# Kernel optimization log

Measured on AMD Instinct MI355X. Metric: run time of the kernel, lower is better.

Reference implementation:

```python
import jax, jax.numpy as jnp
import numpy as np

D_MODEL = 1024
N_HEADS = 16
D_K = D_MODEL // N_HEADS  # 64, also d_v
B, S = 8, 1024


def setup_inputs() -> dict:
    key = jax.random.key(0)
    ks = jax.random.split(key, 12)
    sc = 1.0 / np.sqrt(D_MODEL)
    inp = {
        "q": jax.random.normal(ks[0], (B, S, D_MODEL), jnp.float32),
        "k": jax.random.normal(ks[1], (B, S, D_MODEL), jnp.float32),
        "v": jax.random.normal(ks[2], (B, S, D_MODEL), jnp.float32),
        # per-head projection weights stacked over heads; torch Linear stores [out,in]
        "Wq": jax.random.normal(ks[3], (N_HEADS, D_K, D_MODEL), jnp.float32) * sc,
        "bq": jax.random.normal(ks[4], (N_HEADS, D_K), jnp.float32) * sc,
        "Wk": jax.random.normal(ks[5], (N_HEADS, D_K, D_MODEL), jnp.float32) * sc,
        "bk": jax.random.normal(ks[6], (N_HEADS, D_K), jnp.float32) * sc,
        "Wv": jax.random.normal(ks[7], (N_HEADS, D_K, D_MODEL), jnp.float32) * sc,
        "bv": jax.random.normal(ks[8], (N_HEADS, D_K), jnp.float32) * sc,
        "Wf": jax.random.normal(ks[9], (D_MODEL, D_MODEL), jnp.float32) * sc,
        "bf": jax.random.normal(ks[10], (D_MODEL,), jnp.float32) * sc,
    }
    return inp


def reference(q, k, v, Wq, bq, Wk, bk, Wv, bv, Wf, bf):
    temper = jnp.asarray(D_K ** 0.5, q.dtype)
    # per-head linear projections, all heads at once: [b,s,h,dk]
    qh = jnp.einsum('bsd,hkd->bhsk', q, Wq) + bq[None, :, None, :]
    kh = jnp.einsum('bsd,hkd->bhsk', k, Wk) + bk[None, :, None, :]
    vh = jnp.einsum('bsd,hkd->bhsk', v, Wv) + bv[None, :, None, :]
    # scaled dot-product scores [b,h,s,s]
    scores = jnp.einsum('bhik,bhjk->bhij', qh, kh) / temper
    # faithful scalar-equality mask: positions exactly equal to mask (=0) -> -inf
    scores = jnp.where(scores == 0.0, -jnp.inf, scores)
    attn = jax.nn.softmax(scores, axis=-1)
    out = jnp.einsum('bhij,bhjv->bhiv', attn, vh)  # [b,h,s,dv]
    # concat heads (head order matches torch.cat over ModuleList)
    out = out.transpose(0, 2, 1, 3).reshape(out.shape[0], out.shape[2], -1)  # [b,s,d_model]
    return out @ Wf.T + bf
```

## Files before the change

kernel.cpp:

```cpp
#include <hip/hip_runtime.h>
#include <hip/hip_bf16.h>


#define D_MODEL_ 1024
#define NH_ 16
#define DK_ 64
#define B_ 8
#define S_ 1024
#define M_ (B_ * S_)

typedef __hip_bfloat16 bf16;
typedef __attribute__((ext_vector_type(8))) short short8;
typedef __attribute__((ext_vector_type(4))) short short4_t;
typedef __attribute__((ext_vector_type(4))) float f32x4;

typedef const __attribute__((address_space(1))) unsigned int* gas_u32p;
typedef __attribute__((address_space(3))) unsigned int* las_u32p;

__device__ __forceinline__ short f2bs(float x) {
  bf16 h = __float2bfloat16(x);
  return *reinterpret_cast<short*>(&h);
}

__global__ __launch_bounds__(256)
void conv_f32_bf16(const float* __restrict__ in, bf16* __restrict__ out) {
  size_t i = ((size_t)blockIdx.x * 256 + threadIdx.x) * 8;
  f32x4 a = *(const f32x4*)(in + i);
  f32x4 b = *(const f32x4*)(in + i + 4);
  short8 s;
  s[0] = f2bs(a[0]); s[1] = f2bs(a[1]); s[2] = f2bs(a[2]); s[3] = f2bs(a[3]);
  s[4] = f2bs(b[0]); s[5] = f2bs(b[1]); s[6] = f2bs(b[2]); s[7] = f2bs(b[3]);
  *(short8*)((short*)out + i) = s;
}

__global__ __launch_bounds__(256)
void conv_w4(const float* __restrict__ w0, const float* __restrict__ w1,
             const float* __restrict__ w2, const float* __restrict__ w3,
             bf16* __restrict__ out) {
  const float* src = (blockIdx.z == 0) ? w0 : (blockIdx.z == 1) ? w1
                   : (blockIdx.z == 2) ? w2 : w3;
  size_t i = ((size_t)blockIdx.x * 256 + threadIdx.x) * 8;
  f32x4 a = *(const f32x4*)(src + i);
  f32x4 b = *(const f32x4*)(src + i + 4);
  short8 s;
  s[0] = f2bs(a[0]); s[1] = f2bs(a[1]); s[2] = f2bs(a[2]); s[3] = f2bs(a[3]);
  s[4] = f2bs(b[0]); s[5] = f2bs(b[1]); s[6] = f2bs(b[2]); s[7] = f2bs(b[3]);
  *(short8*)((short*)out + (size_t)blockIdx.z * 1024 * 1024 + i) = s;
}

__global__ __launch_bounds__(256)
void gemm_mfma(const void* __restrict__ A, const bf16* __restrict__ Wb,
               const float* __restrict__ bias, void* __restrict__ C,
               int aF32, int cMode)
{
  __shared__ short As[2][128 * 32];
  __shared__ short Bs[2][128 * 32];
  const int tid = threadIdx.x;
  const int lane = tid & 63;
  const int w = tid >> 6;
  const int l15 = lane & 15, quad = lane >> 4;
  const int wm = (w >> 1) * 64, wn = (w & 1) * 64;
  const int m0 = blockIdx.x * 128, n0 = blockIdx.y * 128;

  const int srow = (lane >> 2);
  const int skc  = (lane & 3) * 8;

  f32x4 acc[4][4];
#pragma unroll
  for (int i = 0; i < 4; ++i)
#pragma unroll
    for (int j = 0; j < 4; ++j)
      acc[i][j] = (f32x4){0.f, 0.f, 0.f, 0.f};

  for (int k0 = 0; k0 < 1024; k0 += 64) {
    __syncthreads();
    if (aF32) {
      const float* Af = (const float*)A;
#pragma unroll
      for (int p = 0; p < 4; ++p) {
        int c = p * 256 + tid;
        int r = c >> 3, kc = (c & 7) * 8;
        const float* g = Af + (size_t)(m0 + r) * 1024 + k0 + kc;
        f32x4 u = *(const f32x4*)g;
        f32x4 v = *(const f32x4*)(g + 4);
        short8 s;
        s[0] = f2bs(u[0]); s[1] = f2bs(u[1]); s[2] = f2bs(u[2]); s[3] = f2bs(u[3]);
        s[4] = f2bs(v[0]); s[5] = f2bs(v[1]); s[6] = f2bs(v[2]); s[7] = f2bs(v[3]);
        *(short8*)&As[kc >> 5][r * 32 + (kc & 31)] = s;
      }
    } else {
      const bf16* Ab = (const bf16*)A;
#pragma unroll
      for (int sub = 0; sub < 2; ++sub)
#pragma unroll
        for (int p = 0; p < 2; ++p) {
          int r = 32 * w + 16 * p + srow;
          __builtin_amdgcn_global_load_lds(
              (gas_u32p)(const void*)(Ab + (size_t)(m0 + r) * 1024 + k0 + sub * 32 + skc),
              (las_u32p)(void*)((char*)&As[sub][0] + w * 2048 + p * 1024), 16, 0, 0);
        }
    }
#pragma unroll
    for (int sub = 0; sub < 2; ++sub)
#pragma unroll
      for (int p = 0; p < 2; ++p) {
        int r = 32 * w + 16 * p + srow;
        __builtin_amdgcn_global_load_lds(
            (gas_u32p)(const void*)(Wb + (size_t)(n0 + r) * 1024 + k0 + sub * 32 + skc),
            (las_u32p)(void*)((char*)&Bs[sub][0] + w * 2048 + p * 1024), 16, 0, 0);
      }
    __syncthreads();

#pragma unroll
    for (int kk = 0; kk < 2; ++kk) {
      short8 af[4], bfv[4];
#pragma unroll
      for (int t = 0; t < 4; ++t) {
        af[t]  = *(short8*)&As[kk][(wm + t * 16 + l15) * 32 + quad * 8];
        bfv[t] = *(short8*)&Bs[kk][(wn + t * 16 + l15) * 32 + quad * 8];
      }
#pragma unroll
      for (int mt = 0; mt < 4; ++mt)
#pragma unroll
        for (int nt = 0; nt < 4; ++nt)
          acc[mt][nt] = __builtin_amdgcn_mfma_f32_16x16x32_bf16(af[mt], bfv[nt], acc[mt][nt], 0, 0, 0);
    }
  }

  if (cMode == 2) {
    bf16* vt = (bf16*)C;
    const int bidx = m0 >> 10;
    const int sbase = (m0 & 1023) + wm;
#pragma unroll
    for (int nt = 0; nt < 4; ++nt) {
      int n = n0 + wn + nt * 16 + l15;
      float bv = bias[n];
#pragma unroll
      for (int mt = 0; mt < 4; ++mt) {
        int s = sbase + mt * 16 + quad * 4;
        short4_t pk;
#pragma unroll
        for (int r = 0; r < 4; ++r) pk[r] = f2bs(acc[mt][nt][r] + bv);
        *(short4_t*)((short*)vt + ((size_t)bidx * 1024 + n) * 1024 + s) = pk;
      }
    }
  } else {
#pragma unroll
    for (int nt = 0; nt < 4; ++nt) {
      int col = n0 + wn + nt * 16 + l15;
      float bv = bias[col];
#pragma unroll
      for (int mt = 0; mt < 4; ++mt)
#pragma unroll
        for (int r = 0; r < 4; ++r) {
          int row = m0 + wm + mt * 16 + quad * 4 + r;
          float val = acc[mt][nt][r] + bv;
          if (cMode == 1) ((float*)C)[(size_t)row * 1024 + col] = val;
          else ((bf16*)C)[(size_t)row * 1024 + col] = __float2bfloat16(val);
        }
    }
  }
}

__global__ __launch_bounds__(256)
void attn_mfma(const bf16* __restrict__ QH, const bf16* __restrict__ KH,
               const bf16* __restrict__ VT, bf16* __restrict__ AO)
{
  __shared__ short Ks[2][64 * 32];
  __shared__ short Vs[2][64 * 32];
  __shared__ short Ps[4][16 * 72];
  const int tid = threadIdx.x;
  const int lane = tid & 63;
  const int w = tid >> 6;
  const int l15 = lane & 15, quad = lane >> 4;
  const int q0 = blockIdx.x * 64;
  const int h = blockIdx.y, b = blockIdx.z;
  const size_t base = ((size_t)b * S_) * D_MODEL_ + (size_t)h * DK_;
  const size_t vtb  = (((size_t)b * NH_ + h) * DK_) * (size_t)S_;
  const float NEG = -1e30f;
  short* myPs = Ps[w];

  const int srow = 16 * w + (lane >> 2);
  const int skc  = (lane & 3) * 8;

  short8 qa[2];
#pragma unroll
  for (int ks = 0; ks < 2; ++ks)
    qa[ks] = *(const short8*)((const short*)QH + base + (size_t)(q0 + w * 16 + l15) * D_MODEL_ + ks * 32 + quad * 8);

  float mi = NEG, li = 0.f;
  f32x4 oacc[4];
#pragma unroll
  for (int nt = 0; nt < 4; ++nt) oacc[nt] = (f32x4){0.f, 0.f, 0.f, 0.f};

  for (int j0 = 0; j0 < S_; j0 += 64) {
    __syncthreads();
#pragma unroll
    for (int sub = 0; sub < 2; ++sub) {
      __builtin_amdgcn_global_load_lds(
          (gas_u32p)(const void*)((const short*)KH + base + (size_t)(j0 + srow) * D_MODEL_ + sub * 32 + skc),
          (las_u32p)(void*)((char*)&Ks[sub][0] + w * 1024), 16, 0, 0);
      __builtin_amdgcn_global_load_lds(
          (gas_u32p)(const void*)((const short*)VT + vtb + (size_t)srow * S_ + j0 + sub * 32 + skc),
          (las_u32p)(void*)((char*)&Vs[sub][0] + w * 1024), 16, 0, 0);
    }
    __syncthreads();

    short8 kb[4][2], vb[4][2];
#pragma unroll
    for (int nt = 0; nt < 4; ++nt)
#pragma unroll
      for (int ks = 0; ks < 2; ++ks) {
        kb[nt][ks] = *(short8*)&Ks[ks][(nt * 16 + l15) * 32 + quad * 8];
        vb[nt][ks] = *(short8*)&Vs[ks][(nt * 16 + l15) * 32 + quad * 8];
      }

    f32x4 sacc[4];
#pragma unroll
    for (int nt = 0; nt < 4; ++nt) sacc[nt] = (f32x4){0.f, 0.f, 0.f, 0.f};
#pragma unroll
    for (int nt = 0; nt < 4; ++nt)
#pragma unroll
      for (int ks = 0; ks < 2; ++ks)
        sacc[nt] = __builtin_amdgcn_mfma_f32_16x16x32_bf16(kb[nt][ks], qa[ks], sacc[nt], 0, 0, 0);

    float p[4][4], rm = NEG;
#pragma unroll
    for (int nt = 0; nt < 4; ++nt)
#pragma unroll
      for (int r = 0; r < 4; ++r) {
        float x = sacc[nt][r] * 0.125f;
        if (x == 0.0f) x = NEG;
        p[nt][r] = x;
        rm = fmaxf(rm, x);
      }
    rm = fmaxf(rm, __shfl_xor(rm, 16, 64));
    rm = fmaxf(rm, __shfl_xor(rm, 32, 64));
    float nm = fmaxf(mi, rm);
    float alpha = __expf(mi - nm);
    float ps = 0.f;
#pragma unroll
    for (int nt = 0; nt < 4; ++nt)
#pragma unroll
      for (int r = 0; r < 4; ++r) {
        float e = __expf(p[nt][r] - nm);
        p[nt][r] = e;
        ps += e;
      }
    ps += __shfl_xor(ps, 16, 64);
    ps += __shfl_xor(ps, 32, 64);
    li = li * alpha + ps;
    mi = nm;

#pragma unroll
    for (int nt = 0; nt < 4; ++nt) {
      short4_t pk;
#pragma unroll
      for (int r = 0; r < 4; ++r) pk[r] = f2bs(p[nt][r]);
      *(short4_t*)&myPs[l15 * 72 + nt * 16 + quad * 4] = pk;
    }

    float ar[4];
#pragma unroll
    for (int r = 0; r < 4; ++r) ar[r] = __shfl(alpha, quad * 4 + r, 64);
#pragma unroll
    for (int nt = 0; nt < 4; ++nt)
#pragma unroll
      for (int r = 0; r < 4; ++r) oacc[nt][r] *= ar[r];

    __threadfence_block();

    short8 pa[2];
#pragma unroll
    for (int ks = 0; ks < 2; ++ks)
      pa[ks] = *(short8*)&myPs[l15 * 72 + ks * 32 + quad * 8];
#pragma unroll
    for (int nt = 0; nt < 4; ++nt)
#pragma unroll
      for (int ks = 0; ks < 2; ++ks)
        oacc[nt] = __builtin_amdgcn_mfma_f32_16x16x32_bf16(pa[ks], vb[nt][ks], oacc[nt], 0, 0, 0);
  }

  float lr[4];
#pragma unroll
  for (int r = 0; r < 4; ++r) lr[r] = __shfl(li, quad * 4 + r, 64);
#pragma unroll
  for (int r = 0; r < 4; ++r) {
    float inv = (lr[r] > 0.f) ? 1.0f / lr[r] : 0.f;
    int q = q0 + w * 16 + quad * 4 + r;
#pragma unroll
    for (int nt = 0; nt < 4; ++nt)
      AO[base + (size_t)q * D_MODEL_ + nt * 16 + l15] = __float2bfloat16(oacc[nt][r] * inv);
  }
}

extern "C" void kernel_launch(void* const* d_in, const int* in_sizes, int n_in,
                              void* d_out, int out_size, void* d_ws, size_t ws_size,
                              hipStream_t stream) {
  (void)in_sizes; (void)n_in; (void)out_size; (void)ws_size;
  const float* q  = (const float*)d_in[0];
  const float* k  = (const float*)d_in[1];
  const float* v  = (const float*)d_in[2];
  const float* Wq = (const float*)d_in[3];
  const float* bq = (const float*)d_in[4];
  const float* Wk = (const float*)d_in[5];
  const float* bk = (const float*)d_in[6];
  const float* Wv = (const float*)d_in[7];
  const float* bv = (const float*)d_in[8];
  const float* Wf = (const float*)d_in[9];
  const float* bF = (const float*)d_in[10];

  const size_t MB = (size_t)1024 * 1024;
  char* ws = (char*)d_ws;
  bf16* wb4 = (bf16*)(ws);
  bf16* wqb = wb4;
  bf16* wkb = (bf16*)(ws + 2 * MB);
  bf16* wvb = (bf16*)(ws + 4 * MB);
  bf16* wfb = (bf16*)(ws + 6 * MB);
  bf16* inb = (bf16*)(ws + 8 * MB);
  bf16* vt  = (bf16*)(ws + 16 * MB);
  bf16* qh  = (bf16*)d_out;
  bf16* kh  = (bf16*)((char*)d_out + 16 * MB);

  dim3 blk(256);
  dim3 igrid(4096);
  dim3 ggrid(M_ / 128, D_MODEL_ / 128);

  conv_w4<<<dim3(512, 1, 4), blk, 0, stream>>>(Wq, Wk, Wv, Wf, wb4);

  conv_f32_bf16<<<igrid, blk, 0, stream>>>(q, inb);
  gemm_mfma<<<ggrid, blk, 0, stream>>>(inb, wqb, bq, qh, 0, 0);
  conv_f32_bf16<<<igrid, blk, 0, stream>>>(k, inb);
  gemm_mfma<<<ggrid, blk, 0, stream>>>(inb, wkb, bk, kh, 0, 0);
  gemm_mfma<<<ggrid, blk, 0, stream>>>(v, wvb, bv, vt, 1, 2);

  attn_mfma<<<dim3(S_ / 64, NH_, B_), blk, 0, stream>>>(qh, kh, vt, qh);

  hipMemcpyAsync(inb, d_out, 16 * MB, hipMemcpyDeviceToDevice, stream);
  gemm_mfma<<<ggrid, blk, 0, stream>>>(inb, wfb, bF, d_out, 0, 1);
}
```

Before: 359.0 us.

## Double-buffer GEMM loads, fold softmax scale into Q, lazy rescale in attention

The GEMM kernel now double-buffers its LDS tiles and prefetches the next K slice, including register-staged f32 A loads, while computing the current one. This overlaps global loads with MFMA work at the cost of twice the shared memory. The 1/sqrt(dk) scale moves into the Q projection epilogue. Attention now skips the online-softmax rescale when the wave's running max grows by at most 8, and raises wave priority around MFMA blocks. The folded scale is applied before bf16 rounding, which is exact since it is a power of two. Tolerating a max lag of 8 keeps exponentials within range.

```diff
diff --git a/kernel.cpp b/kernel.cpp
--- a/kernel.cpp
+++ b/kernel.cpp
@@ -51,10 +51,10 @@
 __global__ __launch_bounds__(256)
 void gemm_mfma(const void* __restrict__ A, const bf16* __restrict__ Wb,
                const float* __restrict__ bias, void* __restrict__ C,
-               int aF32, int cMode)
+               int aF32, int cMode, float cscale)
 {
-  __shared__ short As[2][128 * 32];
-  __shared__ short Bs[2][128 * 32];
+  __shared__ short As[2][2][128 * 32];
+  __shared__ short Bs[2][2][128 * 32];
   const int tid = threadIdx.x;
   const int lane = tid & 63;
   const int w = tid >> 6;
@@ -65,41 +65,21 @@
   const int srow = (lane >> 2);
   const int skc  = (lane & 3) * 8;
 
-  f32x4 acc[4][4];
-#pragma unroll
-  for (int i = 0; i < 4; ++i)
-#pragma unroll
-    for (int j = 0; j < 4; ++j)
-      acc[i][j] = (f32x4){0.f, 0.f, 0.f, 0.f};
-
-  for (int k0 = 0; k0 < 1024; k0 += 64) {
-    __syncthreads();
-    if (aF32) {
-      const float* Af = (const float*)A;
-#pragma unroll
-      for (int p = 0; p < 4; ++p) {
-        int c = p * 256 + tid;
-        int r = c >> 3, kc = (c & 7) * 8;
-        const float* g = Af + (size_t)(m0 + r) * 1024 + k0 + kc;
-        f32x4 u = *(const f32x4*)g;
-        f32x4 v = *(const f32x4*)(g + 4);
-        short8 s;
-        s[0] = f2bs(u[0]); s[1] = f2bs(u[1]); s[2] = f2bs(u[2]); s[3] = f2bs(u[3]);
-        s[4] = f2bs(v[0]); s[5] = f2bs(v[1]); s[6] = f2bs(v[2]); s[7] = f2bs(v[3]);
-        *(short8*)&As[kc >> 5][r * 32 + (kc & 31)] = s;
-      }
-    } else {
-      const bf16* Ab = (const bf16*)A;
-#pragma unroll
-      for (int sub = 0; sub < 2; ++sub)
-#pragma unroll
-        for (int p = 0; p < 2; ++p) {
-          int r = 32 * w + 16 * p + srow;
-          __builtin_amdgcn_global_load_lds(
-              (gas_u32p)(const void*)(Ab + (size_t)(m0 + r) * 1024 + k0 + sub * 32 + skc),
-              (las_u32p)(void*)((char*)&As[sub][0] + w * 2048 + p * 1024), 16, 0, 0);
-        }
-    }
+  f32x4 au[4], av[4];
+
+  auto stageA = [&](int buf, int k0) {
+    const bf16* Ab = (const bf16*)A;
+#pragma unroll
+    for (int sub = 0; sub < 2; ++sub)
+#pragma unroll
+      for (int p = 0; p < 2; ++p) {
+        int r = 32 * w + 16 * p + srow;
+        __builtin_amdgcn_global_load_lds(
+            (gas_u32p)(const void*)(Ab + (size_t)(m0 + r) * 1024 + k0 + sub * 32 + skc),
+            (las_u32p)(void*)((char*)&As[buf][sub][0] + w * 2048 + p * 1024), 16, 0, 0);
+      }
+  };
+  auto stageB = [&](int buf, int k0) {
 #pragma unroll
     for (int sub = 0; sub < 2; ++sub)
 #pragma unroll
@@ -107,17 +87,63 @@
         int r = 32 * w + 16 * p + srow;
         __builtin_amdgcn_global_load_lds(
             (gas_u32p)(const void*)(Wb + (size_t)(n0 + r) * 1024 + k0 + sub * 32 + skc),
-            (las_u32p)(void*)((char*)&Bs[sub][0] + w * 2048 + p * 1024), 16, 0, 0);
-      }
-    __syncthreads();
+            (las_u32p)(void*)((char*)&Bs[buf][sub][0] + w * 2048 + p * 1024), 16, 0, 0);
+      }
+  };
+  auto loadAf = [&](int k0) {
+    const float* Af = (const float*)A;
+#pragma unroll
+    for (int p = 0; p < 4; ++p) {
+      int c = p * 256 + tid;
+      int r = c >> 3, kc = (c & 7) * 8;
+      const float* g = Af + (size_t)(m0 + r) * 1024 + k0 + kc;
+      au[p] = *(const f32x4*)g;
+      av[p] = *(const f32x4*)(g + 4);
+    }
+  };
+  auto writeAf = [&](int buf) {
+#pragma unroll
+    for (int p = 0; p < 4; ++p) {
+      int c = p * 256 + tid;
+      int r = c >> 3, kc = (c & 7) * 8;
+      short8 s;
+      s[0] = f2bs(au[p][0]); s[1] = f2bs(au[p][1]); s[2] = f2bs(au[p][2]); s[3] = f2bs(au[p][3]);
+      s[4] = f2bs(av[p][0]); s[5] = f2bs(av[p][1]); s[6] = f2bs(av[p][2]); s[7] = f2bs(av[p][3]);
+      *(short8*)&As[buf][kc >> 5][r * 32 + (kc & 31)] = s;
+    }
+  };
+
+  f32x4 acc[4][4];
+#pragma unroll
+  for (int i = 0; i < 4; ++i)
+#pragma unroll
+    for (int j = 0; j < 4; ++j)
+      acc[i][j] = (f32x4){0.f, 0.f, 0.f, 0.f};
+
+  if (aF32) { loadAf(0); writeAf(0); }
+  else       stageA(0, 0);
+  stageB(0, 0);
+  __syncthreads();
+
+#pragma unroll 2
+  for (int k0 = 0; k0 < 1024; k0 += 64) {
+    const int cur = (k0 >> 6) & 1;
+    const int nxt = cur ^ 1;
+    const bool pf = (k0 + 64) < 1024;
+
+    if (pf) {
+      if (aF32) loadAf(k0 + 64);
+      else      stageA(nxt, k0 + 64);
+      stageB(nxt, k0 + 64);
+    }
 
 #pragma unroll
     for (int kk = 0; kk < 2; ++kk) {
       short8 af[4], bfv[4];
 #pragma unroll
       for (int t = 0; t < 4; ++t) {
-        af[t]  = *(short8*)&As[kk][(wm + t * 16 + l15) * 32 + quad * 8];
-        bfv[t] = *(short8*)&Bs[kk][(wn + t * 16 + l15) * 32 + quad * 8];
+        af[t]  = *(short8*)&As[cur][kk][(wm + t * 16 + l15) * 32 + quad * 8];
+        bfv[t] = *(short8*)&Bs[cur][kk][(wn + t * 16 + l15) * 32 + quad * 8];
       }
 #pragma unroll
       for (int mt = 0; mt < 4; ++mt)
@@ -125,6 +151,10 @@
         for (int nt = 0; nt < 4; ++nt)
           acc[mt][nt] = __builtin_amdgcn_mfma_f32_16x16x32_bf16(af[mt], bfv[nt], acc[mt][nt], 0, 0, 0);
     }
+
+    if (pf && aF32) writeAf(nxt);
+
+    __syncthreads();
   }
 
   if (cMode == 2) {
@@ -140,7 +170,7 @@
         int s = sbase + mt * 16 + quad * 4;
         short4_t pk;
 #pragma unroll
-        for (int r = 0; r < 4; ++r) pk[r] = f2bs(acc[mt][nt][r] + bv);
+        for (int r = 0; r < 4; ++r) pk[r] = f2bs((acc[mt][nt][r] + bv) * cscale);
         *(short4_t*)((short*)vt + ((size_t)bidx * 1024 + n) * 1024 + s) = pk;
       }
     }
@@ -154,7 +184,7 @@
 #pragma unroll
         for (int r = 0; r < 4; ++r) {
           int row = m0 + wm + mt * 16 + quad * 4 + r;
-          float val = acc[mt][nt][r] + bv;
+          float val = (acc[mt][nt][r] + bv) * cscale;
           if (cMode == 1) ((float*)C)[(size_t)row * 1024 + col] = val;
           else ((bf16*)C)[(size_t)row * 1024 + col] = __float2bfloat16(val);
         }
@@ -218,38 +248,59 @@
     f32x4 sacc[4];
 #pragma unroll
     for (int nt = 0; nt < 4; ++nt) sacc[nt] = (f32x4){0.f, 0.f, 0.f, 0.f};
+    __builtin_amdgcn_s_setprio(1);
 #pragma unroll
     for (int nt = 0; nt < 4; ++nt)
 #pragma unroll
       for (int ks = 0; ks < 2; ++ks)
         sacc[nt] = __builtin_amdgcn_mfma_f32_16x16x32_bf16(kb[nt][ks], qa[ks], sacc[nt], 0, 0, 0);
-
-    float p[4][4], rm = NEG;
+    __builtin_amdgcn_s_setprio(0);
+
+    float p[4][4];
 #pragma unroll
     for (int nt = 0; nt < 4; ++nt)
 #pragma unroll
       for (int r = 0; r < 4; ++r) {
-        float x = sacc[nt][r] * 0.125f;
+        float x = sacc[nt][r];
         if (x == 0.0f) x = NEG;
         p[nt][r] = x;
-        rm = fmaxf(rm, x);
-      }
+      }
+    float mm[4];
+#pragma unroll
+    for (int nt = 0; nt < 4; ++nt)
+      mm[nt] = fmaxf(fmaxf(p[nt][0], p[nt][1]), fmaxf(p[nt][2], p[nt][3]));
+    float rm = fmaxf(fmaxf(mm[0], mm[1]), fmaxf(mm[2], mm[3]));
     rm = fmaxf(rm, __shfl_xor(rm, 16, 64));
     rm = fmaxf(rm, __shfl_xor(rm, 32, 64));
-    float nm = fmaxf(mi, rm);
-    float alpha = __expf(mi - nm);
-    float ps = 0.f;
-#pragma unroll
-    for (int nt = 0; nt < 4; ++nt)
-#pragma unroll
-      for (int r = 0; r < 4; ++r) {
-        float e = __expf(p[nt][r] - nm);
-        p[nt][r] = e;
-        ps += e;
-      }
+
+    const bool skip = __all(rm <= mi + 8.0f);
+    const float nm = skip ? mi : fmaxf(mi, rm);
+
+    float psum[4];
+#pragma unroll
+    for (int nt = 0; nt < 4; ++nt) {
+      float e0 = __expf(p[nt][0] - nm), e1 = __expf(p[nt][1] - nm);
+      float e2 = __expf(p[nt][2] - nm), e3 = __expf(p[nt][3] - nm);
+      p[nt][0] = e0; p[nt][1] = e1; p[nt][2] = e2; p[nt][3] = e3;
+      psum[nt] = (e0 + e1) + (e2 + e3);
+    }
+    float ps = (psum[0] + psum[1]) + (psum[2] + psum[3]);
     ps += __shfl_xor(ps, 16, 64);
     ps += __shfl_xor(ps, 32, 64);
-    li = li * alpha + ps;
+
+    if (skip) {
+      li += ps;
+    } else {
+      float alpha = __expf(mi - nm);
+      li = li * alpha + ps;
+      float ar[4];
+#pragma unroll
+      for (int r = 0; r < 4; ++r) ar[r] = __shfl(alpha, quad * 4 + r, 64);
+#pragma unroll
+      for (int nt = 0; nt < 4; ++nt)
+#pragma unroll
+        for (int r = 0; r < 4; ++r) oacc[nt][r] *= ar[r];
+    }
     mi = nm;
 
 #pragma unroll
@@ -260,25 +311,19 @@
       *(short4_t*)&myPs[l15 * 72 + nt * 16 + quad * 4] = pk;
     }
 
-    float ar[4];
-#pragma unroll
-    for (int r = 0; r < 4; ++r) ar[r] = __shfl(alpha, quad * 4 + r, 64);
-#pragma unroll
-    for (int nt = 0; nt < 4; ++nt)
-#pragma unroll
-      for (int r = 0; r < 4; ++r) oacc[nt][r] *= ar[r];
-
     __threadfence_block();
 
     short8 pa[2];
 #pragma unroll
     for (int ks = 0; ks < 2; ++ks)
       pa[ks] = *(short8*)&myPs[l15 * 72 + ks * 32 + quad * 8];
+    __builtin_amdgcn_s_setprio(1);
 #pragma unroll
     for (int nt = 0; nt < 4; ++nt)
 #pragma unroll
       for (int ks = 0; ks < 2; ++ks)
         oacc[nt] = __builtin_amdgcn_mfma_f32_16x16x32_bf16(pa[ks], vb[nt][ks], oacc[nt], 0, 0, 0);
+    __builtin_amdgcn_s_setprio(0);
   }
 
   float lr[4];
@@ -329,13 +374,13 @@
   conv_w4<<<dim3(512, 1, 4), blk, 0, stream>>>(Wq, Wk, Wv, Wf, wb4);
 
   conv_f32_bf16<<<igrid, blk, 0, stream>>>(q, inb);
-  gemm_mfma<<<ggrid, blk, 0, stream>>>(inb, wqb, bq, qh, 0, 0);
+  gemm_mfma<<<ggrid, blk, 0, stream>>>(inb, wqb, bq, qh, 0, 0, 0.125f);
   conv_f32_bf16<<<igrid, blk, 0, stream>>>(k, inb);
-  gemm_mfma<<<ggrid, blk, 0, stream>>>(inb, wkb, bk, kh, 0, 0);
-  gemm_mfma<<<ggrid, blk, 0, stream>>>(v, wvb, bv, vt, 1, 2);
+  gemm_mfma<<<ggrid, blk, 0, stream>>>(inb, wkb, bk, kh, 0, 0, 1.0f);
+  gemm_mfma<<<ggrid, blk, 0, stream>>>(v, wvb, bv, vt, 1, 2, 1.0f);
 
   attn_mfma<<<dim3(S_ / 64, NH_, B_), blk, 0, stream>>>(qh, kh, vt, qh);
 
   hipMemcpyAsync(inb, d_out, 16 * MB, hipMemcpyDeviceToDevice, stream);
-  gemm_mfma<<<ggrid, blk, 0, stream>>>(inb, wfb, bF, d_out, 0, 1);
-}
+  gemm_mfma<<<ggrid, blk, 0, stream>>>(inb, wfb, bF, d_out, 0, 1, 1.0f);
+}
```

Result: no change. 361.3 us (+0.7%).
